# Kernel optimization log

Hardware: AMD Instinct MI355X
Metric: run time of the kernel (lower is better)

## Reference

```python
import jax, jax.numpy as jnp
import numpy as np

N_CHANNELS = 32
DIM_CAPSULE = 16


def setup_inputs() -> dict:
    key = jax.random.key(0)
    k1, k2, k3 = jax.random.split(key, 3)
    B, H, W, Cin = 32, 56, 56, 256
    d, n = DIM_CAPSULE, N_CHANNELS
    inputs = jax.random.normal(k1, (B, H, W, Cin), dtype=jnp.float32)
    # glorot-ish scale for the 3x3 conv kernel
    convW_1 = jax.random.normal(k2, (3, 3, Cin, d * n), dtype=jnp.float32) * 0.02
    bias_1 = jnp.zeros((d * n,), dtype=jnp.float32)
    CapsAct_W = jax.random.normal(k3, (1, 1, d, d * n), dtype=jnp.float32) * 0.1
    CapsAct_B = jnp.zeros((d * n,), dtype=jnp.float32)
    return {"inputs": inputs, "convW_1": convW_1, "bias_1": bias_1,
            "CapsAct_W": CapsAct_W, "CapsAct_B": CapsAct_B}


def reference(inputs, convW_1, bias_1, CapsAct_W, CapsAct_B):
    d, n = DIM_CAPSULE, N_CHANNELS
    # 3x3 stride-2 SAME conv (NHWC / HWIO), bias, relu
    y = jax.lax.conv_general_dilated(
        inputs, convW_1, window_strides=(2, 2), padding="SAME",
        dimension_numbers=("NHWC", "HWIO", "NHWC"))
    y = jax.nn.relu(y + bias_1)                      # [B, Ho, Wo, d*n]
    B, Ho, Wo, _ = y.shape
    # Per-channel 1x1 convs == grouped matmul over capsule channels.
    yg = y.reshape(B, Ho, Wo, n, d)                  # group channels: [B,Ho,Wo,n,d_in]
    Wg = CapsAct_W.reshape(d, n, d)                  # [d_in, n, d_out]
    bg = CapsAct_B.reshape(n, d)                     # [n, d_out]
    # output layout matches tf: [B, Ho, Wo, dim_capsule, n_channels]
    out = jnp.einsum("bhwnd,dne->bhwen", yg, Wg) + bg.T[None, None, None]
    return out
```

## Files before the change

### kernel.cpp

```cpp
#include <hip/hip_runtime.h>
#include <hip/hip_bf16.h>

typedef __attribute__((ext_vector_type(4))) float f32x4;
typedef __attribute__((ext_vector_type(8))) short s16x8;
typedef __attribute__((ext_vector_type(8))) unsigned short u16x8;
typedef __attribute__((ext_vector_type(4))) unsigned short u16x4;

__device__ __forceinline__ unsigned short bfbits(float f) {
  unsigned int u = __builtin_bit_cast(unsigned int, f);
  return (unsigned short)((u + 0x8000u) >> 16);
}

__device__ __forceinline__ void gll16(void* lds, const void* g) {
  __builtin_amdgcn_global_load_lds(
      (const __attribute__((address_space(1))) unsigned int*)g,
      (__attribute__((address_space(3))) unsigned int*)lds, 16, 0, 0);
}

__global__ __launch_bounds__(256)
void prep_all(const float* __restrict__ in, __hip_bfloat16* __restrict__ dst,
              const float* __restrict__ w, __hip_bfloat16* __restrict__ wt) {
  int t = threadIdx.x;
  if (blockIdx.x < 1824) {
    __shared__ __align__(16) unsigned short row[14848];
    int bh = blockIdx.x;
    int h = bh % 57, b = bh / 57;
    __hip_bfloat16* d = (__hip_bfloat16*)dst + (long)bh * 14848;
    if (h < 56) {
      if (t < 64) {
        int par = t >> 5, cq = t & 31;
        u16x4 z = {0, 0, 0, 0};
        *(u16x4*)(row + (par * 32 + cq) * 232 + 224) = z;
        *(u16x4*)(row + (par * 32 + cq) * 232 + 228) = z;
      }
      const float* src = in + (long)(b * 56 + h) * 56 * 256;
#pragma unroll
      for (int j = 0; j < 14; ++j) {
        int idx = j * 256 + t;
        f32x4 v = *(const f32x4*)(src + idx * 4);
        int e0 = idx * 4;
        int ww = e0 >> 8, c = e0 & 255;
        int off = ((ww & 1) * 32 + (c >> 3)) * 232 + (ww >> 1) * 8 + (c & 7);
        u16x4 q = {bfbits(v[0]), bfbits(v[1]), bfbits(v[2]), bfbits(v[3])};
        *(u16x4*)(row + off) = q;
      }
      __syncthreads();
      for (int i = t; i < 1856; i += 256)
        *(u16x8*)(d + i * 8) = *(const u16x8*)(row + i * 8);
    } else {
      u16x8 z = {0, 0, 0, 0, 0, 0, 0, 0};
      for (int i = t; i < 1856; i += 256) *(u16x8*)(d + i * 8) = z;
    }
  } else {
    int u = (blockIdx.x - 1824) * 256 + t;
    int n = u & 511;
    int c8 = (u >> 9) & 31;
    int kpos = u >> 14;
    int tt = kpos * 8 + (c8 >> 2);
    int cq = c8 & 3;
    const float* src = w + ((kpos * 256 + c8 * 8) * 512) + n;
    u16x8 d;
#pragma unroll
    for (int j = 0; j < 8; ++j) d[j] = bfbits(src[j * 512]);
    int nb = n >> 7, nl = n & 127;
    *reinterpret_cast<u16x8*>(wt + ((tt * 4 + nb) * 4096 + cq * 1024 + nl * 8)) = d;
  }
}

__global__ __launch_bounds__(256, 2)
void caps_main_fast(const __hip_bfloat16* __restrict__ inp,
                    const __hip_bfloat16* __restrict__ wt,
                    const float* __restrict__ bias1,
                    const float* __restrict__ capsW,
                    const float* __restrict__ capsB,
                    float* __restrict__ out) {
  __shared__ __align__(16) unsigned char smem[73728];
  __hip_bfloat16* smem_e = (__hip_bfloat16*)smem;

  int bid = (int)blockIdx.x;
  bid = (bid & 7) * 49 + (bid >> 3);
  int mblk = bid >> 2;
  int nb = bid & 3;
  int p0 = mblk * 256;

  int tid = threadIdx.x;
  int lane = tid & 63;
  int wv = tid >> 6;
  int wm2 = (wv >> 1) * 128;
  int wn = (wv & 1) * 64;
  int col = lane & 15;
  int lq = lane >> 4;

  int baseA[4];
#pragma unroll
  for (int pb = 0; pb < 4; ++pb) {
    int p = p0 + pb * 64 + lane;
    int b = p / 784;
    int rr = p - b * 784;
    int ho = rr / 28;
    int wo = rr - ho * 28;
    baseA[pb] = b * 846336 + 2 * ho * 14848 + wo * 8;
  }

  const __hip_bfloat16* wtb = wt + nb * 4096;

  f32x4 acc[8][4] = {};

  auto stage = [&](int buf, int t) {
    int kp = t >> 3, tc = t & 7;
    int kh = (kp * 11) >> 5;
    int kw = kp - kh * 3;
    int koff = kh * 14848 + (kw & 1) * 7424 + (kw >> 1) * 8 + (tc * 4 + wv) * 232;
    __hip_bfloat16* sa = smem_e + buf * 12288;
#pragma unroll
    for (int pb = 0; pb < 4; ++pb)
      gll16(sa + wv * 2048 + pb * 512, inp + baseA[pb] + koff);
    __hip_bfloat16* sb = sa + 8192;
    const __hip_bfloat16* bs = wtb + t * 16384 + wv * 1024 + lane * 8;
    gll16(sb + wv * 1024, bs);
    gll16(sb + wv * 1024 + 512, bs + 512);
  };

  stage(0, 0);
  stage(1, 1);
  __asm__ volatile("s_waitcnt vmcnt(6)" ::: "memory");
  __builtin_amdgcn_s_barrier();
  __asm__ volatile("" ::: "memory");

  int rd = 0;
  for (int t = 0; t < 72; ++t) {
    if (t + 2 < 72) {
      int st = rd + 2; if (st >= 3) st -= 3;
      stage(st, t + 2);
    }
    const __hip_bfloat16* sa = smem_e + rd * 12288;
    const __hip_bfloat16* sb = sa + 8192;
    s16x8 af[8], bq[4];
#pragma unroll
    for (int mf = 0; mf < 8; ++mf)
      af[mf] = *(const s16x8*)(sa + lq * 2048 + (wm2 + 16 * mf + col) * 8);
#pragma unroll
    for (int nf = 0; nf < 4; ++nf)
      bq[nf] = *(const s16x8*)(sb + lq * 1024 + (wn + 16 * nf + col) * 8);
    __builtin_amdgcn_s_setprio(1);
#pragma unroll
    for (int mf = 0; mf < 8; ++mf)
#pragma unroll
      for (int nf = 0; nf < 4; ++nf)
        acc[mf][nf] = __builtin_amdgcn_mfma_f32_16x16x32_bf16(
            af[mf], bq[nf], acc[mf][nf], 0, 0, 0);
    __builtin_amdgcn_s_setprio(0);
    if (t < 70) {
      __asm__ volatile("s_waitcnt vmcnt(6)" ::: "memory");
    } else if (t == 70) {
      __asm__ volatile("s_waitcnt vmcnt(0)" ::: "memory");
    }
    __builtin_amdgcn_s_barrier();
    __asm__ volatile("" ::: "memory");
    rd = (rd + 1 == 3) ? 0 : rd + 1;
  }

  int gb = nb * 8 + (wv & 1) * 4;
  s16x8 wf[4];
  f32x4 cinit[4];
#pragma unroll
  for (int g = 0; g < 4; ++g) {
    int gg = gb + g;
    s16x8 bw = {0, 0, 0, 0, 0, 0, 0, 0};
    if (lq < 2) {
#pragma unroll
      for (int j = 0; j < 8; ++j)
        bw[j] = (short)bfbits(capsW[(8 * lq + j) * 512 + gg * 16 + col]);
    }
    wf[g] = bw;
    float cb = capsB[gg * 16 + col];
    cinit[g] = f32x4{cb, cb, cb, cb};
  }
  float b1v[4];
  int nBase = nb * 128 + wn;
#pragma unroll
  for (int nf = 0; nf < 4; ++nf) b1v[nf] = bias1[nBase + nf * 16 + col];

  __asm__ volatile("s_waitcnt vmcnt(0) lgkmcnt(0)" ::: "memory");
  __builtin_amdgcn_s_barrier();
  __asm__ volatile("" ::: "memory");

  __hip_bfloat16* yw = smem_e + wv * 8192;
#pragma unroll
  for (int nf = 0; nf < 4; ++nf) {
#pragma unroll
    for (int mf = 0; mf < 8; ++mf) {
      f32x4 a = acc[mf][nf];
#pragma unroll
      for (int r = 0; r < 4; ++r) {
        int pl = mf * 16 + lq * 4 + r;
        int nl = nf * 16 + col;
        float v = a[r] + b1v[nf];
        v = v > 0.f ? v : 0.f;
        int off = (pl * 128 + nl * 2) ^ ((pl & 7) << 4);
        *(unsigned short*)((char*)yw + off) = bfbits(v);
      }
    }
  }
  __asm__ volatile("s_waitcnt lgkmcnt(0)" ::: "memory");

#pragma unroll
  for (int mf = 0; mf < 8; ++mf) {
    int prow = 16 * mf + col;
    f32x4 dd[4];
#pragma unroll
    for (int g = 0; g < 4; ++g) {
      s16x8 afv = {0, 0, 0, 0, 0, 0, 0, 0};
      if (lq < 2) {
        int off = (prow * 128 + g * 32 + lq * 16) ^ ((prow & 7) << 4);
        afv = *(const s16x8*)((char*)yw + off);
      }
      dd[g] = __builtin_amdgcn_mfma_f32_16x16x32_bf16(afv, wf[g], cinit[g], 0, 0, 0);
    }
    long pgl = (long)(p0 + wm2) + 16 * mf;
#pragma unroll
    for (int r = 0; r < 4; ++r) {
      long pg = pgl + 4 * lq + r;
      f32x4 o = {dd[0][r], dd[1][r], dd[2][r], dd[3][r]};
      *(f32x4*)(out + (pg * 16 + col) * 32 + gb) = o;
    }
  }
}

__global__ __launch_bounds__(256, 3)
void caps_main_v1(const float* __restrict__ in, const __hip_bfloat16* __restrict__ wt,
                  const float* __restrict__ bias1, const float* __restrict__ capsW,
                  const float* __restrict__ capsB, float* __restrict__ out) {
  __shared__ __align__(16) unsigned char smem[32768];
  __hip_bfloat16* sA = (__hip_bfloat16*)smem;
  __hip_bfloat16* sB = (__hip_bfloat16*)(smem + 8192);

  int bid = (int)blockIdx.x;
  bid = (bid & 7) * 98 + (bid >> 3);
  int mblk = bid >> 2;
  int nb = bid & 3;
  int p0 = mblk * 128;

  int tid = threadIdx.x;
  int lane = tid & 63;
  int wv = tid >> 6;
  int wm = (wv >> 1) * 64;
  int wn = (wv & 1) * 64;
  int col = lane & 15;
  int lq = lane >> 4;

  int am = tid & 127;
  int ah = tid >> 7;
  int p = p0 + am;
  int bb = p / 784;
  int rr = p - bb * 784;
  int ho = rr / 28;
  int wo = rr - ho * 28;

  f32x4 acc[4][4] = {};
  const __hip_bfloat16* wtb = wt + nb * 4096;

  for (int kp = 0; kp < 9; ++kp) {
    int kh = kp / 3;
    int kw = kp - kh * 3;
    int h = 2 * ho + kh, ww = 2 * wo + kw;
    bool valid = (h < 56) && (ww < 56);
    const float* arow = in + (((bb * 56 + h) * 56 + ww) * 256) + ah * 16;
#pragma unroll
    for (int tc = 0; tc < 8; ++tc) {
      int t = kp * 8 + tc;
      __syncthreads();
      const __hip_bfloat16* bsrc = wtb + t * 16384 + tid * 8;
      gll16(sB + (wv * 512), bsrc);
      gll16(sB + 2048 + (wv * 512), bsrc + 2048);
      f32x4 v0, v1, v2, v3;
      if (valid) {
        const f32x4* apv = (const f32x4*)(arow + tc * 32);
        v0 = apv[0]; v1 = apv[1]; v2 = apv[2]; v3 = apv[3];
      } else {
        v0 = f32x4{0.f, 0.f, 0.f, 0.f}; v1 = v0; v2 = v0; v3 = v0;
      }
      u16x8 pk0, pk1;
#pragma unroll
      for (int j = 0; j < 4; ++j) {
        pk0[j] = bfbits(v0[j]); pk0[j + 4] = bfbits(v1[j]);
        pk1[j] = bfbits(v2[j]); pk1[j + 4] = bfbits(v3[j]);
      }
      *(u16x8*)(sA + (ah * 2) * 1024 + am * 8) = pk0;
      *(u16x8*)(sA + (ah * 2 + 1) * 1024 + am * 8) = pk1;
      __syncthreads();
      s16x8 af[4], bfr[4];
#pragma unroll
      for (int mf = 0; mf < 4; ++mf)
        af[mf] = *(const s16x8*)(sA + lq * 1024 + (wm + 16 * mf + col) * 8);
#pragma unroll
      for (int nf = 0; nf < 4; ++nf)
        bfr[nf] = *(const s16x8*)(sB + lq * 1024 + (wn + 16 * nf + col) * 8);
#pragma unroll
      for (int mf = 0; mf < 4; ++mf)
#pragma unroll
        for (int nf = 0; nf < 4; ++nf)
          acc[mf][nf] = __builtin_amdgcn_mfma_f32_16x16x32_bf16(
              af[mf], bfr[nf], acc[mf][nf], 0, 0, 0);
    }
  }

  __syncthreads();

  __hip_bfloat16* yw = (__hip_bfloat16*)smem + wv * 4096;
  int nBase = nb * 128 + wn;
#pragma unroll
  for (int nf = 0; nf < 4; ++nf) {
    float b1v = bias1[nBase + nf * 16 + col];
#pragma unroll
    for (int mf = 0; mf < 4; ++mf) {
      f32x4 a = acc[mf][nf];
#pragma unroll
      for (int r = 0; r < 4; ++r) {
        int pl = mf * 16 + lq * 4 + r;
        int nl = nf * 16 + col;
        float v = a[r] + b1v;
        v = v > 0.f ? v : 0.f;
        int off = (pl * 128 + nl * 2) ^ ((pl & 7) << 4);
        *(unsigned short*)((char*)yw + off) = bfbits(v);
      }
    }
  }

  int gb = nb * 8 + (wv & 1) * 4;
  s16x8 wf[4];
  f32x4 cinit[4];
#pragma unroll
  for (int g = 0; g < 4; ++g) {
    int gg = gb + g;
    s16x8 bw = {0, 0, 0, 0, 0, 0, 0, 0};
    if (lq < 2) {
#pragma unroll
      for (int j = 0; j < 8; ++j)
        bw[j] = (short)bfbits(capsW[(8 * lq + j) * 512 + gg * 16 + col]);
    }
    wf[g] = bw;
    float cb = capsB[gg * 16 + col];
    cinit[g] = f32x4{cb, cb, cb, cb};
  }
#pragma unroll
  for (int mf = 0; mf < 4; ++mf) {
    int prow = 16 * mf + col;
    f32x4 dd[4];
#pragma unroll
    for (int g = 0; g < 4; ++g) {
      s16x8 afv = {0, 0, 0, 0, 0, 0, 0, 0};
      if (lq < 2) {
        int off = (prow * 128 + g * 32 + lq * 16) ^ ((prow & 7) << 4);
        afv = *(const s16x8*)((char*)yw + off);
      }
      dd[g] = __builtin_amdgcn_mfma_f32_16x16x32_bf16(afv, wf[g], cinit[g], 0, 0, 0);
    }
    long pgl = (long)(p0 + wm) + 16 * mf;
#pragma unroll
    for (int r = 0; r < 4; ++r) {
      long pg = pgl + 4 * lq + r;
      f32x4 o = {dd[0][r], dd[1][r], dd[2][r], dd[3][r]};
      *(f32x4*)(out + (pg * 16 + col) * 32 + gb) = o;
    }
  }
}

extern "C" void kernel_launch(void* const* d_in, const int* in_sizes, int n_in,
                              void* d_out, int out_size, void* d_ws, size_t ws_size,
                              hipStream_t stream) {
  const float* inputs = (const float*)d_in[0];
  const float* convW  = (const float*)d_in[1];
  const float* bias1  = (const float*)d_in[2];
  const float* capsW  = (const float*)d_in[3];
  const float* capsB  = (const float*)d_in[4];
  float* out = (float*)d_out;

  __hip_bfloat16* wt = (__hip_bfloat16*)d_ws;
  const size_t IN_OFF = 2621440;
  const size_t NEED = IN_OFF + (size_t)27082752 * 2;

  if (ws_size >= NEED) {
    __hip_bfloat16* inp = (__hip_bfloat16*)((char*)d_ws + IN_OFF);
    prep_all<<<2400, 256, 0, stream>>>(inputs, inp, convW, wt);
    caps_main_fast<<<392, 256, 0, stream>>>(inp, wt, bias1, capsW, capsB, out);
  } else {
    prep_all<<<2400, 256, 0, stream>>>(inputs, (__hip_bfloat16*)d_ws, convW, wt);
    caps_main_v1<<<784, 256, 0, stream>>>(inputs, wt, bias1, capsW, capsB, out);
  }
}
```

Measured before the change: 99.46 us.

## Load B weight fragments directly to registers instead of staging via LDS

The weight (B) tiles are now read from global memory straight into registers, one step ahead, using a ping-pong register pair. Only the A (input) tiles still go through the triple-buffered LDS ring, which cuts shared memory per block and removes the LDS round trip for B. The trade-off is that each wave issues its own global reads of B, with no sharing through LDS, plus extra register pressure. The vmcnt wait thresholds are retuned for the different number of outstanding loads, and the loop is manually unrolled by two.

```diff
diff --git a/kernel.cpp b/kernel.cpp
--- a/kernel.cpp
+++ b/kernel.cpp
@@ -74,7 +74,7 @@
                     const float* __restrict__ capsW,
                     const float* __restrict__ capsB,
                     float* __restrict__ out) {
-  __shared__ __align__(16) unsigned char smem[73728];
+  __shared__ __align__(16) unsigned char smem[65536];
   __hip_bfloat16* smem_e = (__hip_bfloat16*)smem;
 
   int bid = (int)blockIdx.x;
@@ -103,61 +103,75 @@
   }
 
   const __hip_bfloat16* wtb = wt + nb * 4096;
+  int boff[4];
+#pragma unroll
+  for (int nf = 0; nf < 4; ++nf)
+    boff[nf] = lq * 1024 + (wn + 16 * nf + col) * 8;
 
   f32x4 acc[8][4] = {};
 
-  auto stage = [&](int buf, int t) {
+  auto stageA = [&](int buf, int t) {
     int kp = t >> 3, tc = t & 7;
     int kh = (kp * 11) >> 5;
     int kw = kp - kh * 3;
     int koff = kh * 14848 + (kw & 1) * 7424 + (kw >> 1) * 8 + (tc * 4 + wv) * 232;
-    __hip_bfloat16* sa = smem_e + buf * 12288;
+    __hip_bfloat16* sa = smem_e + buf * 8192;
 #pragma unroll
     for (int pb = 0; pb < 4; ++pb)
       gll16(sa + wv * 2048 + pb * 512, inp + baseA[pb] + koff);
-    __hip_bfloat16* sb = sa + 8192;
-    const __hip_bfloat16* bs = wtb + t * 16384 + wv * 1024 + lane * 8;
-    gll16(sb + wv * 1024, bs);
-    gll16(sb + wv * 1024 + 512, bs + 512);
   };
 
-  stage(0, 0);
-  stage(1, 1);
-  __asm__ volatile("s_waitcnt vmcnt(6)" ::: "memory");
+  auto loadB = [&](int t, s16x8 (&bn)[4]) {
+    const __hip_bfloat16* bg = wtb + t * 16384;
+#pragma unroll
+    for (int nf = 0; nf < 4; ++nf)
+      bn[nf] = *(const s16x8*)(bg + boff[nf]);
+  };
+
+  s16x8 bqA[4], bqB[4];
+
+  stageA(0, 0);
+  stageA(1, 1);
+  loadB(0, bqA);
+  __asm__ volatile("s_waitcnt vmcnt(8)" ::: "memory");
   __builtin_amdgcn_s_barrier();
   __asm__ volatile("" ::: "memory");
 
   int rd = 0;
-  for (int t = 0; t < 72; ++t) {
+  auto STEP = [&](int t, s16x8 (&cur)[4], s16x8 (&nxt)[4]) {
+    if (t + 1 < 72) loadB(t + 1, nxt);
+    __builtin_amdgcn_sched_barrier(0);
+    const __hip_bfloat16* sa = smem_e + rd * 8192;
+    s16x8 af[8];
+#pragma unroll
+    for (int mf = 0; mf < 8; ++mf)
+      af[mf] = *(const s16x8*)(sa + lq * 2048 + (wm2 + 16 * mf + col) * 8);
     if (t + 2 < 72) {
       int st = rd + 2; if (st >= 3) st -= 3;
-      stage(st, t + 2);
-    }
-    const __hip_bfloat16* sa = smem_e + rd * 12288;
-    const __hip_bfloat16* sb = sa + 8192;
-    s16x8 af[8], bq[4];
-#pragma unroll
-    for (int mf = 0; mf < 8; ++mf)
-      af[mf] = *(const s16x8*)(sa + lq * 2048 + (wm2 + 16 * mf + col) * 8);
-#pragma unroll
-    for (int nf = 0; nf < 4; ++nf)
-      bq[nf] = *(const s16x8*)(sb + lq * 1024 + (wn + 16 * nf + col) * 8);
+      stageA(st, t + 2);
+    }
     __builtin_amdgcn_s_setprio(1);
 #pragma unroll
     for (int mf = 0; mf < 8; ++mf)
 #pragma unroll
       for (int nf = 0; nf < 4; ++nf)
         acc[mf][nf] = __builtin_amdgcn_mfma_f32_16x16x32_bf16(
-            af[mf], bq[nf], acc[mf][nf], 0, 0, 0);
+            af[mf], cur[nf], acc[mf][nf], 0, 0, 0);
     __builtin_amdgcn_s_setprio(0);
     if (t < 70) {
-      __asm__ volatile("s_waitcnt vmcnt(6)" ::: "memory");
+      __asm__ volatile("s_waitcnt vmcnt(8)" ::: "memory");
     } else if (t == 70) {
-      __asm__ volatile("s_waitcnt vmcnt(0)" ::: "memory");
+      __asm__ volatile("s_waitcnt vmcnt(4)" ::: "memory");
     }
     __builtin_amdgcn_s_barrier();
     __asm__ volatile("" ::: "memory");
     rd = (rd + 1 == 3) ? 0 : rd + 1;
+  };
+
+#pragma unroll 1
+  for (int t = 0; t < 72; t += 2) {
+    STEP(t, bqA, bqB);
+    STEP(t + 1, bqB, bqA);
   }
 
   int gb = nb * 8 + (wv & 1) * 4;
```

Measured after the change: 108.0 us. 1.09x slower.
